# Optimization experiments

Measured on AMD Instinct MI355X. Metric: run time of the kernel, lower is better.

The kernel has to match this reference:

```python
import jax, jax.numpy as jnp
import numpy as np

K = 4  # knn_graph(k=4, loop=False) hard-coded in H2GCN.forward


def _knn_2hop_adj(Fet, k):
    """Per-batch kNN graph -> symmetrize -> 2-hop binary adjacency [B,N,N].

    Matches create_adj + get_2hop_neighbors: edge direction and the row
    normalization in create_adj are irrelevant because get_2hop_neighbors
    symmetrizes (adj[row,col]=adj[col,row]=1) and thresholds (adj@adj > 0).
    """
    B, N, _ = Fet.shape
    sq = jnp.sum(Fet * Fet, axis=-1)  # [B,N]
    dist = sq[:, :, None] + sq[:, None, :] - 2.0 * jnp.einsum('bnf,bmf->bnm', Fet, Fet)
    eye = jnp.eye(N, dtype=bool)
    dist = jnp.where(eye[None], jnp.inf, dist)  # loop=False: exclude self
    _, idx = jax.lax.top_k(-dist, k)  # [B,N,k] nearest-neighbor indices
    b_idx = jnp.arange(B)[:, None, None]
    n_idx = jnp.arange(N)[None, :, None]
    A = jnp.zeros((B, N, N), Fet.dtype).at[b_idx, n_idx, idx].set(1.0)
    A = jnp.maximum(A, jnp.swapaxes(A, 1, 2))  # symmetrize 1-hop
    A2 = jnp.einsum('bnm,bmk->bnk', A, A)      # 2-hop counts
    A2 = jnp.where(eye[None], 0.0, A2)          # fill_diagonal_(0)
    return (A2 > 0).astype(Fet.dtype)


def _h2gcn_conv(x, A2, w1, b1, w2, b2):
    """H2GCNConv on dense binary adjacency.

    Dense matmul with binary A2 == gather(x[col]) -> fc2 -> index_add over rows;
    A2.sum(-1) == bincount(row). Degree clamped to >= 1.
    """
    ego = jnp.einsum('bnf,of->bno', x, w1) + b1   # fc1(x)
    msg = jnp.einsum('bnf,of->bno', x, w2) + b2   # fc2(x)
    agg = jnp.einsum('bnm,bmo->bno', A2, msg)     # scatter-add of neighbor msgs
    deg = jnp.maximum(jnp.sum(A2, axis=-1, keepdims=True), 1.0)
    return jax.nn.relu(jnp.concatenate([ego, agg / deg], axis=-1))


def setup_inputs() -> dict:
    key = jax.random.key(0)
    ks = jax.random.split(key, 8)
    B, N, F, NH, NC = 128, 197, 768, 512, 1000
    s = 0.02
    return {
        'Fet': jax.random.normal(ks[0], (B, N, F), jnp.float32),
        'w1_0': jax.random.normal(ks[1], (NH, F), jnp.float32) * s,
        'b1_0': jnp.zeros((NH,), jnp.float32),
        'w2_0': jax.random.normal(ks[2], (NH, F), jnp.float32) * s,
        'b2_0': jnp.zeros((NH,), jnp.float32),
        'w1_1': jax.random.normal(ks[3], (NH, 2 * NH), jnp.float32) * s,
        'b1_1': jnp.zeros((NH,), jnp.float32),
        'w2_1': jax.random.normal(ks[4], (NH, 2 * NH), jnp.float32) * s,
        'b2_1': jnp.zeros((NH,), jnp.float32),
        'fc1_w': jax.random.normal(ks[5], (NH, 4 * NH), jnp.float32) * s,
        'fc1_b': jnp.zeros((NH,), jnp.float32),
        'fc2_w': jax.random.normal(ks[6], (NC, NH), jnp.float32) * s,
        'fc2_b': jnp.zeros((NC,), jnp.float32),
    }


def reference(Fet, w1_0, b1_0, w2_0, b2_0, w1_1, b1_1, w2_1, b2_1,
              fc1_w, fc1_b, fc2_w, fc2_b):
    A2 = _knn_2hop_adj(Fet, K)
    h1 = _h2gcn_conv(Fet, A2, w1_0, b1_0, w2_0, b2_0)   # [B,N,2*nhid]
    h2 = _h2gcn_conv(h1, A2, w1_1, b1_1, w2_1, b2_1)    # [B,N,2*nhid]
    h = jnp.concatenate([h1, h2], axis=-1)              # [B,N,final_dim]
    graph_features = jnp.mean(h, axis=1)                # global_mean_pool
    p = jax.nn.relu(graph_features @ fc1_w.T + fc1_b)   # dropout is identity (eval)
    out = p @ fc2_w.T + fc2_b
    return (out, graph_features)
```

## Files before the change

kernel.cpp:

```cpp
#include <hip/hip_runtime.h>
#include <hip/hip_bf16.h>
#include <math.h>

typedef __attribute__((ext_vector_type(8))) short bf16x8;
typedef __attribute__((ext_vector_type(4))) float f32x4;

#define B_ 128
#define N_ 197
#define F_ 768
#define NH_ 512
#define D2_ 1024
#define D4_ 2048
#define NC_ 1000
#define ROWS_ (B_ * N_)
#define KA_ 224
#define NA_ 256
#define LDG_ 200
#define MT_LD_ (B_ * KA_)

#define OFF_G0     0ull
#define OFF_SQ     20172800ull
#define OFF_ABITS  20273664ull
#define OFF_DEG    21080576ull
#define OFF_FETHI  21181440ull
#define OFF_MSGT   60011520ull
#define OFF_H1     89371648ull
#define OFF_FETLO  OFF_MSGT
#define OFF_POOL   141014016ull
#define OFF_P      142062592ull
#define OFF_WC1    142324736ull
#define OFF_WC2    143897600ull
#define OFF_G1     145994752ull

__device__ __forceinline__ void gll16(const void* g, void* l) {
  __builtin_amdgcn_global_load_lds((const __attribute__((address_space(1))) void*)g,
                                   (__attribute__((address_space(3))) void*)l, 16, 0, 0);
}

__device__ __forceinline__ int slot_of(int row) { return (row & 3) ^ ((row >> 2) & 3); }

__global__ __launch_bounds__(256) void cast_weights(const float* __restrict__ w10,
                                                    const float* __restrict__ w20,
                                                    const float* __restrict__ w11,
                                                    const float* __restrict__ w21,
                                                    __hip_bfloat16* __restrict__ wc1,
                                                    __hip_bfloat16* __restrict__ wc2) {
  const int S1 = NH_ * F_ / 4;
  const int S2 = NH_ * D2_ / 4;
  int i = blockIdx.x * 256 + threadIdx.x;
  const float* src;
  __hip_bfloat16* dst;
  int off;
  if (i < S1) { src = w10; dst = wc1; off = i; }
  else if (i < 2 * S1) { src = w20; dst = wc1 + (size_t)NH_ * F_; off = i - S1; }
  else if (i < 2 * S1 + S2) { src = w11; dst = wc2; off = i - 2 * S1; }
  else { src = w21; dst = wc2 + (size_t)NH_ * D2_; off = i - 2 * S1 - S2; }
  float4 v = ((const float4*)src)[off];
  union { __hip_bfloat16 h[4]; uint2 u; } pk;
  pk.h[0] = __float2bfloat16(v.x);
  pk.h[1] = __float2bfloat16(v.y);
  pk.h[2] = __float2bfloat16(v.z);
  pk.h[3] = __float2bfloat16(v.w);
  ((uint2*)dst)[off] = pk.u;
}

__global__ __launch_bounds__(256) void cast_hilo_sq(const float* __restrict__ X,
                                                    __hip_bfloat16* __restrict__ hi,
                                                    __hip_bfloat16* __restrict__ lo,
                                                    float* __restrict__ sq) {
  int row = blockIdx.x * 4 + (threadIdx.x >> 6);
  int lane = threadIdx.x & 63;
  const float4* xp = (const float4*)(X + (size_t)row * F_);
  uint2* hp = (uint2*)(hi + (size_t)row * F_);
  uint2* lp = (uint2*)(lo + (size_t)row * F_);
  float s = 0.f;
#pragma unroll
  for (int i = 0; i < 3; i++) {
    float4 v = xp[lane + i * 64];
    s += v.x * v.x + v.y * v.y + v.z * v.z + v.w * v.w;
    float f[4] = {v.x, v.y, v.z, v.w};
    union { __hip_bfloat16 h[4]; uint2 u; } ph, pl;
#pragma unroll
    for (int k = 0; k < 4; k++) {
      __hip_bfloat16 h = __float2bfloat16(f[k]);
      ph.h[k] = h;
      pl.h[k] = __float2bfloat16(f[k] - __bfloat162float(h));
    }
    hp[lane + i * 64] = ph.u;
    lp[lane + i * 64] = pl.u;
  }
#pragma unroll
  for (int o = 32; o > 0; o >>= 1) s += __shfl_down(s, o);
  if (lane == 0) sq[row] = s;
}

__global__ __launch_bounds__(256) void mfma_gram(const __hip_bfloat16* __restrict__ Xhi,
                                                 const __hip_bfloat16* __restrict__ Xlo,
                                                 float* __restrict__ g0,
                                                 float* __restrict__ g1) {
  __shared__ short AsH[4096];
  __shared__ short BsH[4096];
  __shared__ short AsL[4096];
  __shared__ short BsL[4096];
  const int t = threadIdx.x;
  const int wgid = blockIdx.x;
  const int L = (wgid & 7) * 96 + (wgid >> 3);
  const int b = L / 6;
  const int rbx = L - b * 6;
  const int bx = rbx % 3;
  const int khalf = rbx / 3;
  const int m0 = (bx == 0) ? 0 : 128;
  const int o0 = (bx == 2) ? 128 : 0;
  const bool mirror = (bx == 1);
  const int l = t & 63, w = t >> 6;
  const int wm = (w >> 1) * 64, wn = (w & 1) * 64;
  const int frow = l & 15, fch = l >> 4;
  const int srow = t >> 2, sslot = t & 3;
  const size_t rowbase = (size_t)b * N_;
  const char* AhiB = (const char*)(Xhi + (rowbase + m0) * F_);
  const char* AloB = (const char*)(Xlo + (rowbase + m0) * F_);
  const char* BhiB = (const char*)(Xhi + (rowbase + o0) * F_);
  const char* BloB = (const char*)(Xlo + (rowbase + o0) * F_);
  const int rb = F_ * 2;
  char* AsHB = (char*)AsH;
  char* BsHB = (char*)BsH;
  char* AsLB = (char*)AsL;
  char* BsLB = (char*)BsL;
  float* go = khalf ? g1 : g0;
  f32x4 zero = {0.f, 0.f, 0.f, 0.f};
  f32x4 acc[4][4];
#pragma unroll
  for (int i = 0; i < 4; i++)
#pragma unroll
    for (int j = 0; j < 4; j++) acc[i][j] = zero;
  const int kt0 = khalf * 12;
  for (int kt = kt0; kt < kt0 + 12; kt++) {
    const int kb = kt * 64;
#pragma unroll
    for (int u = 0; u < 2; u++) {
      int grow = u * 64 + srow;
      int gslot = sslot ^ slot_of(grow);
      size_t goff = (size_t)grow * rb + kb + gslot * 16;
      gll16(AhiB + goff, AsHB + u * 4096 + t * 16);
      gll16(BhiB + goff, BsHB + u * 4096 + t * 16);
      gll16(AloB + goff, AsLB + u * 4096 + t * 16);
      gll16(BloB + goff, BsLB + u * 4096 + t * 16);
    }
    __syncthreads();
    bf16x8 ah[4], al[4], bh[4], bl[4];
#pragma unroll
    for (int i = 0; i < 4; i++) {
      int ar = wm + i * 16 + frow;
      int aoff = ar * 64 + ((fch ^ slot_of(ar)) * 16);
      ah[i] = *(const bf16x8*)(AsHB + aoff);
      al[i] = *(const bf16x8*)(AsLB + aoff);
      int br = wn + i * 16 + frow;
      int boff = br * 64 + ((fch ^ slot_of(br)) * 16);
      bh[i] = *(const bf16x8*)(BsHB + boff);
      bl[i] = *(const bf16x8*)(BsLB + boff);
    }
#pragma unroll
    for (int i = 0; i < 4; i++)
#pragma unroll
      for (int j = 0; j < 4; j++) {
        acc[i][j] = __builtin_amdgcn_mfma_f32_16x16x32_bf16(bh[j], ah[i], acc[i][j], 0, 0, 0);
        acc[i][j] = __builtin_amdgcn_mfma_f32_16x16x32_bf16(bl[j], ah[i], acc[i][j], 0, 0, 0);
        acc[i][j] = __builtin_amdgcn_mfma_f32_16x16x32_bf16(bh[j], al[i], acc[i][j], 0, 0, 0);
      }
    __syncthreads();
  }
#pragma unroll
  for (int i = 0; i < 4; i++) {
    int n = m0 + wm + i * 16 + frow;
    if (n >= N_) continue;
    float* gr = go + (rowbase + n) * LDG_;
#pragma unroll
    for (int j = 0; j < 4; j++) {
      int mb = o0 + wn + j * 16 + fch * 4;
      if (mb >= LDG_) continue;
      f32x4 pv = acc[i][j];
      *(f32x4*)&gr[mb] = pv;
      if (mirror) {
#pragma unroll
        for (int r = 0; r < 4; r++)
          go[(rowbase + mb + r) * LDG_ + n] = pv[r];
      }
    }
  }
}

__global__ __launch_bounds__(256) void topk_kernel(const float* __restrict__ g0,
                                                   const float* __restrict__ g1,
                                                   const float* __restrict__ sq,
                                                   unsigned long long* __restrict__ Abits) {
  int row = blockIdx.x * 4 + (threadIdx.x >> 6);
  int lane = threadIdx.x & 63;
  int b = row / N_, n = row - b * N_;
  const float* g0r = g0 + (size_t)row * LDG_;
  const float* g1r = g1 + (size_t)row * LDG_;
  const float* sqb = sq + (size_t)b * N_;
  float v[4];
  int vi[4];
#pragma unroll
  for (int i = 0; i < 4; i++) {
    int m = lane + i * 64;
    bool ok = (m < N_) && (m != n);
    v[i] = ok ? (sqb[m] - 2.f * (g0r[m] + g1r[m])) : INFINITY;
    vi[i] = ok ? m : 0x3fffffff;
  }
  unsigned long long nbr[4] = {0ull, 0ull, 0ull, 0ull};
#pragma unroll
  for (int t = 0; t < 4; t++) {
    float bv = v[0];
    int bi = vi[0];
#pragma unroll
    for (int i = 1; i < 4; i++)
      if (v[i] < bv || (v[i] == bv && vi[i] < bi)) { bv = v[i]; bi = vi[i]; }
#pragma unroll
    for (int o = 1; o < 64; o <<= 1) {
      float ov = __shfl_xor(bv, o);
      int oi = __shfl_xor(bi, o);
      if (ov < bv || (ov == bv && oi < bi)) { bv = ov; bi = oi; }
    }
#pragma unroll
    for (int i = 0; i < 4; i++)
      if (vi[i] == bi) { v[i] = INFINITY; vi[i] = 0x3fffffff; }
    if (lane == 0) {
      nbr[bi >> 6] |= 1ull << (bi & 63);
      atomicOr(&Abits[((size_t)b * N_ + bi) * 4 + (n >> 6)], 1ull << (n & 63));
    }
  }
  if (lane == 0) {
#pragma unroll
    for (int w = 0; w < 4; w++)
      if (nbr[w]) atomicOr(&Abits[(size_t)row * 4 + w], nbr[w]);
  }
}

__global__ __launch_bounds__(256) void a2_kernel(const unsigned long long* __restrict__ Abits,
                                                 __hip_bfloat16* __restrict__ A2bf,
                                                 float* __restrict__ deg) {
  int row = blockIdx.x * 4 + (threadIdx.x >> 6);
  int lane = threadIdx.x & 63;
  int b = row / N_, n = row - b * N_;
  const unsigned long long* arow = Abits + (size_t)row * 4;
  const unsigned long long* base = Abits + (size_t)b * N_ * 4;
  unsigned long long r0 = 0, r1 = 0, r2 = 0, r3 = 0;
#pragma unroll
  for (int w = 0; w < 4; w++) {
    if ((arow[w] >> lane) & 1ull) {
      const unsigned long long* mr = base + (size_t)(w * 64 + lane) * 4;
      r0 |= mr[0]; r1 |= mr[1]; r2 |= mr[2]; r3 |= mr[3];
    }
  }
#pragma unroll
  for (int o = 1; o < 64; o <<= 1) {
    r0 |= __shfl_xor(r0, o);
    r1 |= __shfl_xor(r1, o);
    r2 |= __shfl_xor(r2, o);
    r3 |= __shfl_xor(r3, o);
  }
  unsigned long long rr[4] = {r0, r1, r2, r3};
  rr[n >> 6] &= ~(1ull << (n & 63));
  const int pad = b & 3;
  __hip_bfloat16* out = A2bf + ((size_t)b * NA_ + n) * KA_;
  const __hip_bfloat16 one = __float2bfloat16(1.f);
  const __hip_bfloat16 zer = __float2bfloat16(0.f);
#pragma unroll
  for (int i = 0; i < 4; i++) {
    int m = lane + i * 64;
    if (m < KA_) {
      int k = m - pad;
      bool bit = (k >= 0 && k < N_ && ((rr[k >> 6] >> (k & 63)) & 1ull));
      out[m] = bit ? one : zer;
    }
  }
  if (lane == 0) {
    int dg = __popcll(rr[0]) + __popcll(rr[1]) + __popcll(rr[2]) + __popcll(rr[3]);
    deg[row] = (float)(dg > 0 ? dg : 1);
  }
}

template <int MODE>
__global__ __launch_bounds__(256) void mfma_fused(const __hip_bfloat16* __restrict__ X,
                                                  const __hip_bfloat16* __restrict__ Wcat,
                                                  const float* __restrict__ biasE,
                                                  const float* __restrict__ biasM,
                                                  __hip_bfloat16* __restrict__ h1,
                                                  __hip_bfloat16* __restrict__ msgT,
                                                  float* __restrict__ pool,
                                                  int K) {
  __shared__ short As[4096];
  __shared__ short Bs[4096];
  const int t = threadIdx.x;
  const int wgid = blockIdx.x;
  const int L = (wgid & 7) * 197 + (wgid >> 3);
  const int m0 = (L >> 3) * 128, o0 = (L & 7) * 128;
  const int l = t & 63, w = t >> 6;
  const int wm = (w >> 1) * 64, wn = (w & 1) * 64;
  const int frow = l & 15, fch = l >> 4;
  const int srow = t >> 2, sslot = t & 3;
  const char* Abase = (const char*)(X + (size_t)m0 * K);
  const char* Bbase = (const char*)(Wcat + (size_t)o0 * K);
  const int rb = K * 2;
  char* AsB = (char*)As;
  char* BsB = (char*)Bs;
  const bool ego = (o0 < 512);
  const bool swap = (MODE == 1) && ego;
  f32x4 zero = {0.f, 0.f, 0.f, 0.f};
  f32x4 acc[4][4];
#pragma unroll
  for (int i = 0; i < 4; i++)
#pragma unroll
    for (int j = 0; j < 4; j++) acc[i][j] = zero;
  const int KT = K >> 5;
  for (int kt = 0; kt < KT; kt++) {
    const int kb = kt * 64;
#pragma unroll
    for (int u = 0; u < 2; u++) {
      int grow = u * 64 + srow;
      int gslot = sslot ^ slot_of(grow);
      gll16(Abase + (size_t)grow * rb + kb + gslot * 16, AsB + u * 4096 + t * 16);
      gll16(Bbase + (size_t)grow * rb + kb + gslot * 16, BsB + u * 4096 + t * 16);
    }
    __syncthreads();
    bf16x8 af[4], bfv[4];
#pragma unroll
    for (int i = 0; i < 4; i++) {
      int ar = wm + i * 16 + frow;
      af[i] = *(const bf16x8*)(AsB + ar * 64 + ((fch ^ slot_of(ar)) * 16));
      int br = wn + i * 16 + frow;
      bfv[i] = *(const bf16x8*)(BsB + br * 64 + ((fch ^ slot_of(br)) * 16));
    }
    if (!swap) {
#pragma unroll
      for (int i = 0; i < 4; i++)
#pragma unroll
        for (int j = 0; j < 4; j++)
          acc[i][j] = __builtin_amdgcn_mfma_f32_16x16x32_bf16(af[i], bfv[j], acc[i][j], 0, 0, 0);
    } else {
#pragma unroll
      for (int i = 0; i < 4; i++)
#pragma unroll
        for (int j = 0; j < 4; j++)
          acc[i][j] = __builtin_amdgcn_mfma_f32_16x16x32_bf16(bfv[j], af[i], acc[i][j], 0, 0, 0);
    }
    __syncthreads();
  }
  if (ego) {
    if (MODE == 1) {
#pragma unroll
      for (int j = 0; j < 4; j++) {
        int c0 = o0 + wn + j * 16 + fch * 4;
        float4 b4 = *(const float4*)&biasE[c0];
        float bb4[4] = {b4.x, b4.y, b4.z, b4.w};
#pragma unroll
        for (int i = 0; i < 4; i++) {
          int xrow = m0 + wm + i * 16 + frow;
          union { __hip_bfloat16 h[4]; uint2 u; } pk;
#pragma unroll
          for (int r = 0; r < 4; r++)
            pk.h[r] = __float2bfloat16(fmaxf(acc[i][j][r] + bb4[r], 0.f));
          *(uint2*)&h1[(size_t)xrow * D2_ + c0] = pk.u;
        }
      }
    } else {
#pragma unroll
      for (int j = 0; j < 4; j++) {
        int c = o0 + wn + j * 16 + frow;
        float bv = biasE[c];
        int rw = m0 + wm;
        int b0 = rw / N_;
        int rB = (b0 + 1) * N_;
        float sA = 0.f, sB = 0.f;
#pragma unroll
        for (int i = 0; i < 4; i++) {
          int r0 = m0 + wm + i * 16 + fch * 4;
#pragma unroll
          for (int r = 0; r < 4; r++) {
            float v = fmaxf(acc[i][j][r] + bv, 0.f);
            if (r0 + r < rB) sA += v; else sB += v;
          }
        }
        sA += __shfl_down(sA, 32);
        sA += __shfl_down(sA, 16);
        sB += __shfl_down(sB, 32);
        sB += __shfl_down(sB, 16);
        if (l < 16) {
          atomicAdd(&pool[(size_t)b0 * D4_ + D2_ + c], sA);
          if (rw + 64 > rB) atomicAdd(&pool[(size_t)(b0 + 1) * D4_ + D2_ + c], sB);
        }
      }
    }
  } else {
#pragma unroll
    for (int j = 0; j < 4; j++) {
      int cm = (o0 - 512) + wn + j * 16 + frow;
      float bm = biasM[cm];
      __hip_bfloat16* mrow = msgT + (size_t)cm * MT_LD_;
#pragma unroll
      for (int i = 0; i < 4; i++) {
        int x0 = m0 + wm + i * 16 + fch * 4;
        int b0 = x0 / N_;
        int r0 = x0 - b0 * N_;
        union { __hip_bfloat16 h[4]; uint2 u; } pk;
#pragma unroll
        for (int r = 0; r < 4; r++) pk.h[r] = __float2bfloat16(acc[i][j][r] + bm);
        if (r0 + 3 < N_) {
          *(uint2*)&mrow[b0 * KA_ + (b0 & 3) + r0] = pk.u;
        } else {
#pragma unroll
          for (int r = 0; r < 4; r++) {
            int x = x0 + r;
            int bb = x / N_;
            int rx = x - bb * N_;
            mrow[bb * KA_ + (bb & 3) + rx] = pk.h[r];
          }
        }
      }
    }
  }
}

template <int MODE>
__global__ __launch_bounds__(256) void mfma_agg(const __hip_bfloat16* __restrict__ A2bf,
                                                const __hip_bfloat16* __restrict__ msgT,
                                                const float* __restrict__ deg,
                                                __hip_bfloat16* __restrict__ h1,
                                                float* __restrict__ pool, int poolOff) {
  __shared__ short As[4096];
  __shared__ short Bs[4096];
  const int t = threadIdx.x;
  const int wgid = blockIdx.x;
  const int L = (wgid & 7) * 128 + (wgid >> 3);
  const int b = L >> 3;
  const int o0 = ((L >> 1) & 3) * 128;
  const int m0 = (L & 1) * 128;
  const int l = t & 63, w = t >> 6;
  const int wm = (w >> 1) * 64, wn = (w & 1) * 64;
  const int frow = l & 15, fch = l >> 4;
  const int srow = t >> 2, sslot = t & 3;
  const char* Abase = (const char*)(A2bf + ((size_t)b * NA_ + m0) * KA_);
  const char* Bbase = (const char*)(msgT + (size_t)o0 * MT_LD_ + (size_t)b * KA_);
  char* AsB = (char*)As;
  char* BsB = (char*)Bs;
  f32x4 zero = {0.f, 0.f, 0.f, 0.f};
  f32x4 acc[4][4];
#pragma unroll
  for (int i = 0; i < 4; i++)
#pragma unroll
    for (int j = 0; j < 4; j++) acc[i][j] = zero;
  for (int kt = 0; kt < 7; kt++) {
    const int kb = kt * 64;
#pragma unroll
    for (int u = 0; u < 2; u++) {
      int grow = u * 64 + srow;
      int gslot = sslot ^ slot_of(grow);
      gll16(Abase + (size_t)grow * (KA_ * 2) + kb + gslot * 16, AsB + u * 4096 + t * 16);
      gll16(Bbase + (size_t)grow * (MT_LD_ * 2) + kb + gslot * 16, BsB + u * 4096 + t * 16);
    }
    __syncthreads();
    bf16x8 af[4], bfv[4];
#pragma unroll
    for (int i = 0; i < 4; i++) {
      int ar = wm + i * 16 + frow;
      af[i] = *(const bf16x8*)(AsB + ar * 64 + ((fch ^ slot_of(ar)) * 16));
      int br = wn + i * 16 + frow;
      bfv[i] = *(const bf16x8*)(BsB + br * 64 + ((fch ^ slot_of(br)) * 16));
    }
#pragma unroll
    for (int i = 0; i < 4; i++)
#pragma unroll
      for (int j = 0; j < 4; j++)
        acc[i][j] = __builtin_amdgcn_mfma_f32_16x16x32_bf16(bfv[j], af[i], acc[i][j], 0, 0, 0);
    __syncthreads();
  }
  float sv[4][4];
#pragma unroll
  for (int j = 0; j < 4; j++)
#pragma unroll
    for (int r = 0; r < 4; r++) sv[j][r] = 0.f;
#pragma unroll
  for (int i = 0; i < 4; i++) {
    int n = m0 + wm + i * 16 + frow;
    bool ok = (n < N_);
    float dinv = ok ? (1.f / deg[b * N_ + n]) : 0.f;
#pragma unroll
    for (int j = 0; j < 4; j++) {
      int c0 = o0 + wn + j * 16 + fch * 4;
      union { __hip_bfloat16 h[4]; uint2 u; } pk;
#pragma unroll
      for (int r = 0; r < 4; r++) {
        float v = ok ? fmaxf(acc[i][j][r] * dinv, 0.f) : 0.f;
        sv[j][r] += v;
        pk.h[r] = __float2bfloat16(v);
      }
      if (MODE == 0 && ok)
        *(uint2*)&h1[((size_t)b * N_ + n) * D2_ + NH_ + c0] = pk.u;
    }
  }
#pragma unroll
  for (int j = 0; j < 4; j++) {
#pragma unroll
    for (int r = 0; r < 4; r++) {
      float s = sv[j][r];
      s += __shfl_down(s, 8, 16);
      s += __shfl_down(s, 4, 16);
      s += __shfl_down(s, 2, 16);
      s += __shfl_down(s, 1, 16);
      if ((l & 15) == 0)
        atomicAdd(&pool[(size_t)b * D4_ + poolOff + o0 + wn + j * 16 + fch * 4 + r], s);
    }
  }
}

__global__ __launch_bounds__(256) void pool_h1ego(const __hip_bfloat16* __restrict__ h1,
                                                  float* __restrict__ gf) {
  int b = blockIdx.y;
  int c = blockIdx.x * 256 + threadIdx.x;
  const __hip_bfloat16* p = h1 + (size_t)b * N_ * D2_ + c;
  float s = 0.f;
  for (int n = 0; n < N_; n++) s += __bfloat162float(p[(size_t)n * D2_]);
  gf[(size_t)b * D4_ + c] = s * (1.f / N_);
}

__global__ __launch_bounds__(256) void scale_pool(const float* __restrict__ pool,
                                                  float* __restrict__ gf) {
  int b = blockIdx.y;
  int c = NH_ + blockIdx.x * 256 + threadIdx.x;
  gf[(size_t)b * D4_ + c] = pool[(size_t)b * D4_ + c] * (1.f / N_);
}

template <bool RELUX>
__global__ __launch_bounds__(256) void head_gemm(const float* __restrict__ Xg,
                                                 const float* __restrict__ W,
                                                 const float* __restrict__ bias,
                                                 float* __restrict__ Y,
                                                 int Rows, int Fin, int O, int kchunk) {
  __shared__ float Xs[16][68];
  __shared__ float Ws[16][68];
  int tx = threadIdx.x, ty = threadIdx.y;
  int tid = ty * 16 + tx;
  int lr = tid >> 2;
  int lk = (tid & 3) * 4;
  int rbase = blockIdx.y * 64;
  int o0 = blockIdx.x * 64;
  int k0base = blockIdx.z * kchunk;
  float acc[4][4] = {};
  for (int k0 = k0base; k0 < k0base + kchunk; k0 += 16) {
    float4 xv = make_float4(0.f, 0.f, 0.f, 0.f);
    if (rbase + lr < Rows) xv = *(const float4*)&Xg[(size_t)(rbase + lr) * Fin + k0 + lk];
    if (RELUX) {
      xv.x = fmaxf(xv.x, 0.f); xv.y = fmaxf(xv.y, 0.f);
      xv.z = fmaxf(xv.z, 0.f); xv.w = fmaxf(xv.w, 0.f);
    }
    Xs[lk][lr] = xv.x; Xs[lk + 1][lr] = xv.y; Xs[lk + 2][lr] = xv.z; Xs[lk + 3][lr] = xv.w;
    float4 wv = make_float4(0.f, 0.f, 0.f, 0.f);
    if (o0 + lr < O) wv = *(const float4*)&W[(size_t)(o0 + lr) * Fin + k0 + lk];
    Ws[lk][lr] = wv.x; Ws[lk + 1][lr] = wv.y; Ws[lk + 2][lr] = wv.z; Ws[lk + 3][lr] = wv.w;
    __syncthreads();
#pragma unroll
    for (int k = 0; k < 16; k++) {
      float4 a = *(const float4*)&Xs[k][ty * 4];
      float4 bb = *(const float4*)&Ws[k][tx * 4];
      float av[4] = {a.x, a.y, a.z, a.w};
      float bv[4] = {bb.x, bb.y, bb.z, bb.w};
#pragma unroll
      for (int i = 0; i < 4; i++)
#pragma unroll
        for (int j = 0; j < 4; j++) acc[i][j] = fmaf(av[i], bv[j], acc[i][j]);
    }
    __syncthreads();
  }
#pragma unroll
  for (int i = 0; i < 4; i++) {
    int rrow = rbase + ty * 4 + i;
    if (rrow >= Rows) continue;
#pragma unroll
    for (int j = 0; j < 4; j++) {
      int c = o0 + tx * 4 + j;
      if (c >= O) continue;
      float vv = acc[i][j] + ((blockIdx.z == 0) ? bias[c] : 0.f);
      atomicAdd(&Y[(size_t)rrow * O + c], vv);
    }
  }
}

extern "C" void kernel_launch(void* const* d_in, const int* in_sizes, int n_in,
                              void* d_out, int out_size, void* d_ws, size_t ws_size,
                              hipStream_t stream) {
  const float* Fet  = (const float*)d_in[0];
  const float* w1_0 = (const float*)d_in[1];
  const float* b1_0 = (const float*)d_in[2];
  const float* w2_0 = (const float*)d_in[3];
  const float* b2_0 = (const float*)d_in[4];
  const float* w1_1 = (const float*)d_in[5];
  const float* b1_1 = (const float*)d_in[6];
  const float* w2_1 = (const float*)d_in[7];
  const float* b2_1 = (const float*)d_in[8];
  const float* fc1_w = (const float*)d_in[9];
  const float* fc1_b = (const float*)d_in[10];
  const float* fc2_w = (const float*)d_in[11];
  const float* fc2_b = (const float*)d_in[12];

  char* ws = (char*)d_ws;
  float* g0 = (float*)(ws + OFF_G0);
  float* g1 = (float*)(ws + OFF_G1);
  __hip_bfloat16* A2bf = (__hip_bfloat16*)(ws + OFF_G0);
  float* sq = (float*)(ws + OFF_SQ);
  unsigned long long* Abits = (unsigned long long*)(ws + OFF_ABITS);
  float* deg = (float*)(ws + OFF_DEG);
  __hip_bfloat16* Fet_hi = (__hip_bfloat16*)(ws + OFF_FETHI);
  __hip_bfloat16* Fet_lo = (__hip_bfloat16*)(ws + OFF_FETLO);
  __hip_bfloat16* msgT = (__hip_bfloat16*)(ws + OFF_MSGT);
  __hip_bfloat16* h1 = (__hip_bfloat16*)(ws + OFF_H1);
  float* pool = (float*)(ws + OFF_POOL);
  float* p = (float*)(ws + OFF_P);
  __hip_bfloat16* wc1 = (__hip_bfloat16*)(ws + OFF_WC1);
  __hip_bfloat16* wc2 = (__hip_bfloat16*)(ws + OFF_WC2);

  float* out = (float*)d_out;
  float* gf = out + (size_t)B_ * NC_;

  hipMemsetAsync(Abits, 0, (size_t)ROWS_ * 4 * sizeof(unsigned long long), stream);
  hipMemsetAsync(pool, 0, (size_t)B_ * D4_ * sizeof(float), stream);
  hipMemsetAsync(p, 0, (size_t)B_ * NH_ * sizeof(float), stream);
  hipMemsetAsync(out, 0, (size_t)B_ * NC_ * sizeof(float), stream);

  cast_hilo_sq<<<ROWS_ / 4, 256, 0, stream>>>(Fet, Fet_hi, Fet_lo, sq);
  cast_weights<<<1792, 256, 0, stream>>>(w1_0, w2_0, w1_1, w2_1, wc1, wc2);

  mfma_gram<<<768, 256, 0, stream>>>(Fet_hi, Fet_lo, g0, g1);
  topk_kernel<<<ROWS_ / 4, 256, 0, stream>>>(g0, g1, sq, Abits);
  a2_kernel<<<ROWS_ / 4, 256, 0, stream>>>(Abits, A2bf, deg);

  mfma_fused<1><<<1576, 256, 0, stream>>>(Fet_hi, wc1, b1_0, b2_0, h1, msgT, nullptr, F_);
  mfma_agg<0><<<1024, 256, 0, stream>>>(A2bf, msgT, deg, h1, pool, NH_);

  mfma_fused<2><<<1576, 256, 0, stream>>>(h1, wc2, b1_1, b2_1, nullptr, msgT, pool, D2_);
  mfma_agg<1><<<1024, 256, 0, stream>>>(A2bf, msgT, deg, nullptr, pool, D2_ + NH_);

  pool_h1ego<<<dim3(2, B_), 256, 0, stream>>>(h1, gf);
  scale_pool<<<dim3(6, B_), 256, 0, stream>>>(pool, gf);

  head_gemm<false><<<dim3(8, 2, 16), dim3(16, 16), 0, stream>>>(
      gf, fc1_w, fc1_b, p, B_, D4_, NH_, 128);
  head_gemm<true><<<dim3(16, 2, 8), dim3(16, 16), 0, stream>>>(
      p, fc2_w, fc2_b, out, B_, NH_, NC_, 64);
}
```

Baseline: 461.0 us.

## Swizzle LDS with 8-slot XOR layout and fuse h1 ego pooling into GEMM epilogue

Changes the LDS tile layout in the gram, fused and aggregation GEMMs. Two 64-row halves are now interleaved into 128-byte physical rows with an 8-way XOR swizzle, to cut bank conflicts on the fragment reads and to widen the global_load_lds pattern. Separately, the layer-1 ego epilogue now accumulates per-graph column sums, handling tiles that straddle two graphs, and atomically adds them into the pool buffer. This removes the pool_h1ego kernel that re-read h1. The cost is extra shuffles and atomics in the epilogue, and pooling now uses fp32 values rather than the bf16-rounded ones.

```diff
diff --git a/kernel.cpp b/kernel.cpp
--- a/kernel.cpp
+++ b/kernel.cpp
@@ -37,7 +37,6 @@
                                    (__attribute__((address_space(3))) void*)l, 16, 0, 0);
 }
 
-__device__ __forceinline__ int slot_of(int row) { return (row & 3) ^ ((row >> 2) & 3); }
 
 __global__ __launch_bounds__(256) void cast_weights(const float* __restrict__ w10,
                                                     const float* __restrict__ w20,
@@ -115,7 +114,6 @@
   const int l = t & 63, w = t >> 6;
   const int wm = (w >> 1) * 64, wn = (w & 1) * 64;
   const int frow = l & 15, fch = l >> 4;
-  const int srow = t >> 2, sslot = t & 3;
   const size_t rowbase = (size_t)b * N_;
   const char* AhiB = (const char*)(Xhi + (rowbase + m0) * F_);
   const char* AloB = (const char*)(Xlo + (rowbase + m0) * F_);
@@ -138,9 +136,10 @@
     const int kb = kt * 64;
 #pragma unroll
     for (int u = 0; u < 2; u++) {
-      int grow = u * 64 + srow;
-      int gslot = sslot ^ slot_of(grow);
-      size_t goff = (size_t)grow * rb + kb + gslot * 16;
+      int prow = u * 32 + (t >> 3);
+      int e = (t & 7) ^ (prow & 7);
+      int grow = (e >> 2) * 64 + prow;
+      size_t goff = (size_t)grow * rb + kb + (e & 3) * 16;
       gll16(AhiB + goff, AsHB + u * 4096 + t * 16);
       gll16(BhiB + goff, BsHB + u * 4096 + t * 16);
       gll16(AloB + goff, AsLB + u * 4096 + t * 16);
@@ -151,11 +150,13 @@
 #pragma unroll
     for (int i = 0; i < 4; i++) {
       int ar = wm + i * 16 + frow;
-      int aoff = ar * 64 + ((fch ^ slot_of(ar)) * 16);
+      int apr = ar & 63;
+      int aoff = apr * 128 + (((((ar >> 6) << 2) | fch) ^ (apr & 7)) * 16);
       ah[i] = *(const bf16x8*)(AsHB + aoff);
       al[i] = *(const bf16x8*)(AsLB + aoff);
       int br = wn + i * 16 + frow;
-      int boff = br * 64 + ((fch ^ slot_of(br)) * 16);
+      int bpr = br & 63;
+      int boff = bpr * 128 + (((((br >> 6) << 2) | fch) ^ (bpr & 7)) * 16);
       bh[i] = *(const bf16x8*)(BsHB + boff);
       bl[i] = *(const bf16x8*)(BsLB + boff);
     }
@@ -299,7 +300,6 @@
   const int l = t & 63, w = t >> 6;
   const int wm = (w >> 1) * 64, wn = (w & 1) * 64;
   const int frow = l & 15, fch = l >> 4;
-  const int srow = t >> 2, sslot = t & 3;
   const char* Abase = (const char*)(X + (size_t)m0 * K);
   const char* Bbase = (const char*)(Wcat + (size_t)o0 * K);
   const int rb = K * 2;
@@ -318,19 +318,23 @@
     const int kb = kt * 64;
 #pragma unroll
     for (int u = 0; u < 2; u++) {
-      int grow = u * 64 + srow;
-      int gslot = sslot ^ slot_of(grow);
-      gll16(Abase + (size_t)grow * rb + kb + gslot * 16, AsB + u * 4096 + t * 16);
-      gll16(Bbase + (size_t)grow * rb + kb + gslot * 16, BsB + u * 4096 + t * 16);
+      int prow = u * 32 + (t >> 3);
+      int e = (t & 7) ^ (prow & 7);
+      int grow = (e >> 2) * 64 + prow;
+      size_t goff = (size_t)grow * rb + kb + (e & 3) * 16;
+      gll16(Abase + goff, AsB + u * 4096 + t * 16);
+      gll16(Bbase + goff, BsB + u * 4096 + t * 16);
     }
     __syncthreads();
     bf16x8 af[4], bfv[4];
 #pragma unroll
     for (int i = 0; i < 4; i++) {
       int ar = wm + i * 16 + frow;
-      af[i] = *(const bf16x8*)(AsB + ar * 64 + ((fch ^ slot_of(ar)) * 16));
+      int apr = ar & 63;
+      af[i] = *(const bf16x8*)(AsB + apr * 128 + (((((ar >> 6) << 2) | fch) ^ (apr & 7)) * 16));
       int br = wn + i * 16 + frow;
-      bfv[i] = *(const bf16x8*)(BsB + br * 64 + ((fch ^ slot_of(br)) * 16));
+      int bpr = br & 63;
+      bfv[i] = *(const bf16x8*)(BsB + bpr * 128 + (((((br >> 6) << 2) | fch) ^ (bpr & 7)) * 16));
     }
     if (!swap) {
 #pragma unroll
@@ -349,19 +353,39 @@
   }
   if (ego) {
     if (MODE == 1) {
+      const int rw = m0 + wm;
+      const int b0 = rw / N_;
+      const int rloc = (b0 + 1) * N_ - rw;
 #pragma unroll
       for (int j = 0; j < 4; j++) {
         int c0 = o0 + wn + j * 16 + fch * 4;
         float4 b4 = *(const float4*)&biasE[c0];
         float bb4[4] = {b4.x, b4.y, b4.z, b4.w};
+        float sA4[4] = {0.f, 0.f, 0.f, 0.f};
+        float sB4[4] = {0.f, 0.f, 0.f, 0.f};
 #pragma unroll
         for (int i = 0; i < 4; i++) {
-          int xrow = m0 + wm + i * 16 + frow;
+          int xloc = i * 16 + frow;
           union { __hip_bfloat16 h[4]; uint2 u; } pk;
 #pragma unroll
-          for (int r = 0; r < 4; r++)
-            pk.h[r] = __float2bfloat16(fmaxf(acc[i][j][r] + bb4[r], 0.f));
-          *(uint2*)&h1[(size_t)xrow * D2_ + c0] = pk.u;
+          for (int r = 0; r < 4; r++) {
+            float v = fmaxf(acc[i][j][r] + bb4[r], 0.f);
+            pk.h[r] = __float2bfloat16(v);
+            if (xloc < rloc) sA4[r] += v; else sB4[r] += v;
+          }
+          *(uint2*)&h1[(size_t)(rw + xloc) * D2_ + c0] = pk.u;
+        }
+#pragma unroll
+        for (int r = 0; r < 4; r++) {
+          float sA = sA4[r], sB = sB4[r];
+          sA += __shfl_down(sA, 8, 16); sA += __shfl_down(sA, 4, 16);
+          sA += __shfl_down(sA, 2, 16); sA += __shfl_down(sA, 1, 16);
+          sB += __shfl_down(sB, 8, 16); sB += __shfl_down(sB, 4, 16);
+          sB += __shfl_down(sB, 2, 16); sB += __shfl_down(sB, 1, 16);
+          if ((l & 15) == 0) {
+            atomicAdd(&pool[(size_t)b0 * D4_ + c0 + r], sA);
+            if (rloc < 64) atomicAdd(&pool[(size_t)(b0 + 1) * D4_ + c0 + r], sB);
+          }
         }
       }
     } else {
@@ -439,7 +463,6 @@
   const int l = t & 63, w = t >> 6;
   const int wm = (w >> 1) * 64, wn = (w & 1) * 64;
   const int frow = l & 15, fch = l >> 4;
-  const int srow = t >> 2, sslot = t & 3;
   const char* Abase = (const char*)(A2bf + ((size_t)b * NA_ + m0) * KA_);
   const char* Bbase = (const char*)(msgT + (size_t)o0 * MT_LD_ + (size_t)b * KA_);
   char* AsB = (char*)As;
@@ -454,19 +477,22 @@
     const int kb = kt * 64;
 #pragma unroll
     for (int u = 0; u < 2; u++) {
-      int grow = u * 64 + srow;
-      int gslot = sslot ^ slot_of(grow);
-      gll16(Abase + (size_t)grow * (KA_ * 2) + kb + gslot * 16, AsB + u * 4096 + t * 16);
-      gll16(Bbase + (size_t)grow * (MT_LD_ * 2) + kb + gslot * 16, BsB + u * 4096 + t * 16);
+      int prow = u * 32 + (t >> 3);
+      int e = (t & 7) ^ (prow & 7);
+      int grow = (e >> 2) * 64 + prow;
+      gll16(Abase + (size_t)grow * (KA_ * 2) + kb + (e & 3) * 16, AsB + u * 4096 + t * 16);
+      gll16(Bbase + (size_t)grow * (MT_LD_ * 2) + kb + (e & 3) * 16, BsB + u * 4096 + t * 16);
     }
     __syncthreads();
     bf16x8 af[4], bfv[4];
 #pragma unroll
     for (int i = 0; i < 4; i++) {
       int ar = wm + i * 16 + frow;
-      af[i] = *(const bf16x8*)(AsB + ar * 64 + ((fch ^ slot_of(ar)) * 16));
+      int apr = ar & 63;
+      af[i] = *(const bf16x8*)(AsB + apr * 128 + (((((ar >> 6) << 2) | fch) ^ (apr & 7)) * 16));
       int br = wn + i * 16 + frow;
-      bfv[i] = *(const bf16x8*)(BsB + br * 64 + ((fch ^ slot_of(br)) * 16));
+      int bpr = br & 63;
+      bfv[i] = *(const bf16x8*)(BsB + bpr * 128 + (((((br >> 6) << 2) | fch) ^ (bpr & 7)) * 16));
     }
 #pragma unroll
     for (int i = 0; i < 4; i++)
@@ -514,20 +540,10 @@
   }
 }
 
-__global__ __launch_bounds__(256) void pool_h1ego(const __hip_bfloat16* __restrict__ h1,
+__global__ __launch_bounds__(256) void scale_pool(const float* __restrict__ pool,
                                                   float* __restrict__ gf) {
   int b = blockIdx.y;
   int c = blockIdx.x * 256 + threadIdx.x;
-  const __hip_bfloat16* p = h1 + (size_t)b * N_ * D2_ + c;
-  float s = 0.f;
-  for (int n = 0; n < N_; n++) s += __bfloat162float(p[(size_t)n * D2_]);
-  gf[(size_t)b * D4_ + c] = s * (1.f / N_);
-}
-
-__global__ __launch_bounds__(256) void scale_pool(const float* __restrict__ pool,
-                                                  float* __restrict__ gf) {
-  int b = blockIdx.y;
-  int c = NH_ + blockIdx.x * 256 + threadIdx.x;
   gf[(size_t)b * D4_ + c] = pool[(size_t)b * D4_ + c] * (1.f / N_);
 }
 
@@ -634,14 +650,13 @@
   topk_kernel<<<ROWS_ / 4, 256, 0, stream>>>(g0, g1, sq, Abits);
   a2_kernel<<<ROWS_ / 4, 256, 0, stream>>>(Abits, A2bf, deg);
 
-  mfma_fused<1><<<1576, 256, 0, stream>>>(Fet_hi, wc1, b1_0, b2_0, h1, msgT, nullptr, F_);
+  mfma_fused<1><<<1576, 256, 0, stream>>>(Fet_hi, wc1, b1_0, b2_0, h1, msgT, pool, F_);
   mfma_agg<0><<<1024, 256, 0, stream>>>(A2bf, msgT, deg, h1, pool, NH_);
 
   mfma_fused<2><<<1576, 256, 0, stream>>>(h1, wc2, b1_1, b2_1, nullptr, msgT, pool, D2_);
   mfma_agg<1><<<1024, 256, 0, stream>>>(A2bf, msgT, deg, nullptr, pool, D2_ + NH_);
 
-  pool_h1ego<<<dim3(2, B_), 256, 0, stream>>>(h1, gf);
-  scale_pool<<<dim3(6, B_), 256, 0, stream>>>(pool, gf);
+  scale_pool<<<dim3(8, B_), 256, 0, stream>>>(pool, gf);
 
   head_gemm<false><<<dim3(8, 2, 16), dim3(16, 16), 0, stream>>>(
       gf, fc1_w, fc1_b, p, B_, D4_, NH_, 128);
```

After: 444.6 us. -3.6%, faster.
